# Kernel optimization log

Hardware: AMD Instinct MI355X
Metric: run time of the kernel (lower is better)

## Reference

```python
import jax, jax.numpy as jnp
import numpy as np

FREQ_DIM = 32
TIME_DIM = 32
HEADS = 8
TWO_PI = 6.283185307179586


def get_embeddings(B, H, W, freq_dim, time_dim, dtype):
    # freq embeddings over the height (frequency) axis
    nf = freq_dim // 2
    ln_x = jnp.log2(jnp.arange(0, H * nf, dtype=jnp.float32))
    ln_x = ln_x.at[0].set(-2.0)
    ln_x = ln_x.reshape(H, nf).T  # [nf, H]
    ln_x = ln_x * jnp.arange(1, nf + 1, dtype=jnp.float32)[:, None]
    # view_as_real(exp(1j*theta)) -> (cos, sin), interleaved per order along channel dim
    freq = jnp.stack([jnp.cos(ln_x), jnp.sin(ln_x)], axis=1).reshape(freq_dim, H)  # [freq_dim, H]
    freq = jnp.broadcast_to(freq[None, :, :, None], (B, freq_dim, H, W))

    # time embeddings over the width (time) axis
    nt = time_dim // 2
    k = jnp.arange(0, nt, dtype=jnp.float32) + 0.5  # [nt]
    x = jnp.arange(0, nt * W, dtype=jnp.float32).reshape(W, nt).T  # [nt, W]
    theta = k[:, None] * x / (W * nt) * TWO_PI  # [nt, W]
    time = jnp.stack([jnp.cos(theta), jnp.sin(theta)], axis=1).reshape(time_dim, W)  # [time_dim, W]
    time = jnp.broadcast_to(time[None, :, None, :], (B, time_dim, H, W))

    return jnp.concatenate([freq, time], axis=1).astype(dtype)  # [B, freq_dim+time_dim, H, W]


def setup_inputs() -> dict:
    key = jax.random.key(0)
    ks = jax.random.split(key, 6)
    B, C, H, W = 2, 512, 64, 32
    qkC = C + FREQ_DIM + TIME_DIM  # 576
    inner = HEADS * 64  # 512
    return {
        "hidden_states": jax.random.normal(ks[0], (B, C, H, W), dtype=jnp.float32),
        "Wq": jax.random.normal(ks[1], (qkC, inner), dtype=jnp.float32) * 0.02,
        "Wk": jax.random.normal(ks[2], (qkC, inner), dtype=jnp.float32) * 0.02,
        "Wv": jax.random.normal(ks[3], (C, inner), dtype=jnp.float32) * 0.02,
        "Wout": jax.random.normal(ks[4], (inner, C), dtype=jnp.float32) * 0.02,
        "bout": jnp.zeros((C,), dtype=jnp.float32),
    }


def reference(hidden_states, Wq, Wk, Wv, Wout, bout):
    B, C, H, W = hidden_states.shape
    emb = get_embeddings(B, H, W, FREQ_DIM, TIME_DIM, hidden_states.dtype)
    qk_hs = jnp.concatenate([hidden_states, emb], axis=1)  # [B, qkC, H, W]

    S = H * W
    qk_hs = qk_hs.reshape(B, -1, S).transpose(0, 2, 1)  # [B, S, qkC]
    v_hs = hidden_states.reshape(B, C, S).transpose(0, 2, 1)  # [B, S, C]

    q = qk_hs @ Wq  # [B, S, inner]
    k = qk_hs @ Wk
    v = v_hs @ Wv

    hd_qk = q.shape[-1] // HEADS
    hd_v = v.shape[-1] // HEADS
    q = q.reshape(B, S, HEADS, hd_qk).transpose(0, 2, 1, 3)  # [B, h, S, d]
    k = k.reshape(B, S, HEADS, hd_qk).transpose(0, 2, 1, 3)
    v = v.reshape(B, S, HEADS, hd_v).transpose(0, 2, 1, 3)

    scale = 1.0 / jnp.sqrt(jnp.asarray(hd_qk, dtype=q.dtype))
    scores = jnp.einsum('bhqd,bhkd->bhqk', q, k) * scale
    attn = jax.nn.softmax(scores, axis=-1)
    o = jnp.einsum('bhqk,bhkd->bhqd', attn, v)  # [B, h, S, d_v]

    o = o.transpose(0, 2, 1, 3).reshape(B, S, HEADS * hd_v)
    o = o @ Wout + bout  # [B, S, C]
    o = o.transpose(0, 2, 1).reshape(B, C, H, W)

    return o + hidden_states  # residual_connection=True, rescale_output_factor=1.0
```

## Files before the change

kernel.cpp:

```cpp
#include <hip/hip_runtime.h>
#include <math.h>

#define B_    2
#define C_    512
#define H_    64
#define W_    32
#define S_    2048
#define QKC_  576
#define INNER_ 512
#define NH_   8
#define HD_   64
#define TWO_PI_ 6.283185307179586f

typedef __attribute__((ext_vector_type(8))) short bfrag;
typedef __attribute__((ext_vector_type(4))) float ffrag;
typedef __attribute__((ext_vector_type(16))) float f16v;

typedef __attribute__((address_space(1))) const unsigned int as1_u32;
typedef __attribute__((address_space(3))) unsigned int as3_u32;

__device__ __forceinline__ ushort f2bf(float f) {
    unsigned u = __builtin_bit_cast(unsigned, f);
    unsigned r = (u + 0x7FFFu + ((u >> 16) & 1u)) >> 16;
    return (ushort)r;
}

__device__ __forceinline__ f16v zero16() {
    f16v z;
    #pragma unroll
    for (int i = 0; i < 16; i++) z[i] = 0.f;
    return z;
}

#define GLD(gp_, lp_) __builtin_amdgcn_global_load_lds((as1_u32*)(gp_), (as3_u32*)(lp_), 16, 0, 0)

__global__ void k_trans_emb(const float* __restrict__ hid, ushort* __restrict__ X) {
    __shared__ float t[32][33];
    int b  = blockIdx.z;
    int s0 = blockIdx.x * 32, c0 = blockIdx.y * 32;
    int tx = threadIdx.x, ty = threadIdx.y;
    if (c0 < 512) {
        t[ty][tx] = hid[((size_t)b * C_ + (c0 + ty)) * S_ + s0 + tx];
        __syncthreads();
        X[((size_t)(b * S_ + s0 + ty)) * QKC_ + c0 + tx] = f2bf(t[tx][ty]);
    } else {
        int c = c0 - 512 + tx;
        int s = s0 + ty;
        int h = s >> 5, w = s & 31;
        float val;
        if (c < 32) {
            int f = c >> 1;
            int n = h * 16 + f;
            float lx = (n == 0) ? -2.0f : log2f((float)n);
            float arg = lx * (float)(f + 1);
            val = (c & 1) ? sinf(arg) : cosf(arg);
        } else {
            int tt = (c - 32) >> 1;
            float theta = ((float)tt + 0.5f) * (float)(w * 16 + tt) * (TWO_PI_ / 512.0f);
            val = (c & 1) ? sinf(theta) : cosf(theta);
        }
        X[(size_t)(b * S_ + s) * QKC_ + c0 + tx] = f2bf(val);
    }
}

__global__ void k_wtrans_all(const float* __restrict__ Wq, const float* __restrict__ Wk,
                             const float* __restrict__ Wv, const float* __restrict__ Wo,
                             ushort* __restrict__ Wqt, ushort* __restrict__ Wkt,
                             ushort* __restrict__ Wvt, ushort* __restrict__ Wot) {
    __shared__ float t[32][33];
    int z = blockIdx.z;
    const float* W; ushort* Wt; int K;
    if (z == 0)      { W = Wq; Wt = Wqt; K = QKC_; }
    else if (z == 1) { W = Wk; Wt = Wkt; K = QKC_; }
    else if (z == 2) { W = Wv; Wt = Wvt; K = C_; }
    else             { W = Wo; Wt = Wot; K = INNER_; }
    int k0 = blockIdx.x * 32, n0 = blockIdx.y * 32;
    if (k0 >= K) return;
    int tx = threadIdx.x, ty = threadIdx.y;
    t[ty][tx] = W[(size_t)(k0 + ty) * 512 + n0 + tx];
    __syncthreads();
    Wt[(size_t)(n0 + ty) * K + k0 + tx] = f2bf(t[tx][ty]);
}

#define GSTAGE(buf_, k0_) {                                                   \
    _Pragma("unroll")                                                         \
    for (int i_ = 0; i_ < 6; i_++)                                            \
        GLD(gp[i_] + (k0_), tl + (buf_) * 12288 + lo[i_]); }

__global__ __launch_bounds__(256, 3) void k_qkv(const ushort* __restrict__ X,
                                                const ushort* __restrict__ Wqt,
                                                const ushort* __restrict__ Wkt,
                                                const ushort* __restrict__ Wvt,
                                                ushort* __restrict__ Qb,
                                                ushort* __restrict__ Kbb,
                                                ushort* __restrict__ Vtg) {
    __shared__ ushort __attribute__((aligned(16))) tl[2 * 12288];

    int tid = threadIdx.x;
    int l = tid & 63, wv = tid >> 6;
    int wr = wv >> 1, wc = wv & 1;
    int n0 = blockIdx.x * 64, m0 = blockIdx.y * 128;
    int sel = n0 >> 9, n0l = n0 & 511;
    const ushort* Bt = (sel == 0) ? Wqt : (sel == 1) ? Wkt : Wvt;
    const int K = (sel < 2) ? QKC_ : C_;
    const int nst = K >> 6;
    int l15 = l & 15, lg = l >> 4;
    int swz = l15 & 7;

    const ushort* gp[6];
    unsigned lo[6];
    {
        int rsub = l >> 3;
        int clog = (l & 7) ^ rsub;
        #pragma unroll
        for (int i = 0; i < 6; i++) {
            int c = wv * 6 + i;
            lo[i] = c * 512;
            if (c < 16) gp[i] = X  + (size_t)(m0  + c * 8        + rsub) * QKC_ + clog * 8;
            else        gp[i] = Bt + (size_t)(n0l + (c - 16) * 8 + rsub) * K    + clog * 8;
        }
    }

    ffrag acc[4][2];
    #pragma unroll
    for (int i = 0; i < 4; i++)
        #pragma unroll
        for (int j = 0; j < 2; j++) acc[i][j] = (ffrag){0.f, 0.f, 0.f, 0.f};

    GSTAGE(0, 0);
    int cur = 0;
    for (int kt = 0; kt < nst; kt++) {
        __syncthreads();
        if (kt + 1 < nst) GSTAGE(cur ^ 1, (kt + 1) * 64);
        const ushort* As = tl + cur * 12288;
        const ushort* Bs = As + 8192;
        #pragma unroll
        for (int ks = 0; ks < 2; ks++) {
            int cl = ks * 4 + lg;
            int ch = (cl ^ swz) * 8;
            bfrag af[4], bf[2];
            #pragma unroll
            for (int mi = 0; mi < 4; mi++)
                af[mi] = *(const bfrag*)(As + (wr * 64 + mi * 16 + l15) * 64 + ch);
            #pragma unroll
            for (int nj = 0; nj < 2; nj++)
                bf[nj] = *(const bfrag*)(Bs + (wc * 32 + nj * 16 + l15) * 64 + ch);
            #pragma unroll
            for (int mi = 0; mi < 4; mi++)
                #pragma unroll
                for (int nj = 0; nj < 2; nj++)
                    acc[mi][nj] = __builtin_amdgcn_mfma_f32_16x16x32_bf16(af[mi], bf[nj], acc[mi][nj], 0, 0, 0);
        }
        cur ^= 1;
    }

    if (sel < 2) {
        ushort* Co = sel ? Kbb : Qb;
        #pragma unroll
        for (int mi = 0; mi < 4; mi++)
            #pragma unroll
            for (int nj = 0; nj < 2; nj++)
                #pragma unroll
                for (int r = 0; r < 4; r++) {
                    int row = m0 + wr * 64 + mi * 16 + lg * 4 + r;
                    int col = n0l + wc * 32 + nj * 16 + l15;
                    Co[(size_t)row * INNER_ + col] = f2bf(acc[mi][nj][r]);
                }
    } else {
        ushort (*Ct)[136] = (ushort(*)[136])tl;
        __syncthreads();
        #pragma unroll
        for (int mi = 0; mi < 4; mi++)
            #pragma unroll
            for (int nj = 0; nj < 2; nj++)
                #pragma unroll
                for (int r = 0; r < 4; r++)
                    Ct[wc * 32 + nj * 16 + l15][wr * 64 + mi * 16 + lg * 4 + r] = f2bf(acc[mi][nj][r]);
        __syncthreads();
        int b = m0 >> 11, s0m = m0 & 2047;
        #pragma unroll
        for (int p = 0; p < 4; p++) {
            int c = tid + p * 256;
            int rowc = c >> 4, mc = c & 15;
            uint4 v = *(uint4*)&Ct[rowc][mc * 8];
            *(uint4*)(Vtg + (((size_t)(b * 512 + n0l + rowc)) << 11) + s0m + mc * 8) = v;
        }
    }
}

__global__ __launch_bounds__(256, 2) void k_og(const ushort* __restrict__ Ob,
                                               const ushort* __restrict__ Wot,
                                               const float* __restrict__ bias,
                                               const float* __restrict__ hid,
                                               float* __restrict__ out) {
    __shared__ ushort __attribute__((aligned(16))) tl[2 * 12288];

    int tid = threadIdx.x;
    int l = tid & 63, wv = tid >> 6;
    int wr = wv >> 1, wc = wv & 1;
    int n0 = blockIdx.x * 64, m0 = blockIdx.y * 128;
    int l15 = l & 15, lg = l >> 4;
    int swz = l15 & 7;

    const ushort* gp[6];
    unsigned lo[6];
    {
        int rsub = l >> 3;
        int clog = (l & 7) ^ rsub;
        #pragma unroll
        for (int i = 0; i < 6; i++) {
            int c = wv * 6 + i;
            lo[i] = c * 512;
            if (c < 16) gp[i] = Ob  + (size_t)(m0 + c * 8        + rsub) * INNER_ + clog * 8;
            else        gp[i] = Wot + (size_t)(n0 + (c - 16) * 8 + rsub) * INNER_ + clog * 8;
        }
    }

    ffrag acc[4][2];
    #pragma unroll
    for (int i = 0; i < 4; i++)
        #pragma unroll
        for (int j = 0; j < 2; j++) acc[i][j] = (ffrag){0.f, 0.f, 0.f, 0.f};

    GSTAGE(0, 0);
    int cur = 0;
    for (int kt = 0; kt < 8; kt++) {
        __syncthreads();
        if (kt < 7) GSTAGE(cur ^ 1, (kt + 1) * 64);
        const ushort* As = tl + cur * 12288;
        const ushort* Bs = As + 8192;
        #pragma unroll
        for (int ks = 0; ks < 2; ks++) {
            int cl = ks * 4 + lg;
            int ch = (cl ^ swz) * 8;
            bfrag af[4], bf[2];
            #pragma unroll
            for (int mi = 0; mi < 4; mi++)
                af[mi] = *(const bfrag*)(As + (wr * 64 + mi * 16 + l15) * 64 + ch);
            #pragma unroll
            for (int nj = 0; nj < 2; nj++)
                bf[nj] = *(const bfrag*)(Bs + (wc * 32 + nj * 16 + l15) * 64 + ch);
            #pragma unroll
            for (int mi = 0; mi < 4; mi++)
                #pragma unroll
                for (int nj = 0; nj < 2; nj++)
                    acc[mi][nj] = __builtin_amdgcn_mfma_f32_16x16x32_bf16(af[mi], bf[nj], acc[mi][nj], 0, 0, 0);
        }
        cur ^= 1;
    }

    float (*Cf)[129] = (float(*)[129])tl;
    float bv[2];
    #pragma unroll
    for (int nj = 0; nj < 2; nj++) bv[nj] = bias[n0 + wc * 32 + nj * 16 + l15];
    __syncthreads();
    #pragma unroll
    for (int mi = 0; mi < 4; mi++)
        #pragma unroll
        for (int nj = 0; nj < 2; nj++)
            #pragma unroll
            for (int r = 0; r < 4; r++)
                Cf[wc * 32 + nj * 16 + l15][wr * 64 + mi * 16 + lg * 4 + r] = acc[mi][nj][r] + bv[nj];
    __syncthreads();
    int b = m0 >> 11, s0m = m0 & 2047;
    #pragma unroll
    for (int p = 0; p < 8; p++) {
        int f = p * 256 + tid;
        int c = f >> 5, sq = (f & 31) * 4;
        size_t o = (((size_t)(b * 512 + n0 + c)) << 11) + s0m + sq;
        float4 hv = *(const float4*)(hid + o);
        float4 cv = *(float4*)&Cf[c][sq];
        cv.x += hv.x; cv.y += hv.y; cv.z += hv.z; cv.w += hv.w;
        *(float4*)(out + o) = cv;
    }
}

#define CVTPK(dst, a, b) asm("v_cvt_pk_bf16_f32 %0, %1, %2" : "=v"(dst) : "v"(a), "v"(b))
#define SWAP32(a, b)     asm("v_permlane32_swap_b32 %0, %1" : "+v"(a), "+v"(b))

#define STAGE(buf_, kt_) {                                                    \
    const ushort* g_ = gsrc + (size_t)(kt_) * ktstride;                       \
    ushort* lp_ = ktv + (buf_) * 16384 + wv * 4096;                           \
    _Pragma("unroll")                                                         \
    for (int i_ = 0; i_ < 8; i_++)                                            \
        GLD(g_ + (size_t)i_ * istride, lp_ + i_ * 512); }

__global__ __launch_bounds__(256, 2) void k_attn(const ushort* __restrict__ Qf,
                                                 const ushort* __restrict__ Kf,
                                                 const ushort* __restrict__ Vtg,
                                                 ushort* __restrict__ Ob) {
    __shared__ ushort __attribute__((aligned(16))) ktv[2 * 4 * 4096];
    __shared__ float mlsh[2][2][2][32];

    const int qb = blockIdx.x, hd = blockIdx.y, b = blockIdx.z;
    const int tid = threadIdx.x;
    const int l = tid & 63, wv = tid >> 6;
    const int wp = wv >> 1, hh = wv & 1;
    const int l31 = l & 31, hi = l >> 5, swz = l31 & 7;
    const int hoff = hd * HD_;
    const int brow = b * S_ + qb * 64;

    bfrag qf[4];
    {
        const ushort* qp = Qf + (size_t)(brow + wp * 32 + l31) * INNER_ + hoff + hi * 8;
        #pragma unroll
        for (int ks = 0; ks < 4; ks++) qf[ks] = *(const bfrag*)(qp + ks * 16);
    }

    const int hv = wv >> 1, isV = wv & 1;
    const int rr = l >> 3;
    const int clog = (l & 7) ^ rr;
    const ushort* gsrc;
    size_t istride, ktstride;
    if (isV) {
        gsrc = Vtg + (size_t)(b * 512 + hoff + rr) * 2048 + hv * 1024 + clog * 8;
        istride = (size_t)8 * 2048;
        ktstride = 64;
    } else {
        gsrc = Kf + (size_t)(b * S_ + hv * 1024 + rr) * INNER_ + hoff + clog * 8;
        istride = (size_t)8 * INNER_;
        ktstride = (size_t)64 * INNER_;
    }

    STAGE(0, 0);

    float m_run = -INFINITY, l_run = 0.f;
    f16v acc0 = zero16(), acc1 = zero16();
    int cur = 0;

    for (int kt = 0; kt < 16; kt++) {
        __syncthreads();
        if (kt < 15) STAGE(cur ^ 1, kt + 1);

        const ushort* Kt  = ktv + cur * 16384 + hh * 8192;
        const ushort* Vtt = Kt + 4096;

        f16v sf0 = zero16(), sf1 = zero16();
        #pragma unroll
        for (int ks = 0; ks < 4; ks++) {
            int ch = ((ks * 2 + hi) ^ swz) * 8;
            bfrag k0 = *(const bfrag*)(Kt + l31 * 64 + ch);
            bfrag k1 = *(const bfrag*)(Kt + (l31 + 32) * 64 + ch);
            sf0 = __builtin_amdgcn_mfma_f32_32x32x16_bf16(k0, qf[ks], sf0, 0, 0, 0);
            sf1 = __builtin_amdgcn_mfma_f32_32x32x16_bf16(k1, qf[ks], sf1, 0, 0, 0);
        }

        float tm = -INFINITY;
        #pragma unroll
        for (int j = 0; j < 16; j++) { tm = fmaxf(tm, sf0[j]); tm = fmaxf(tm, sf1[j]); }
        tm = fmaxf(tm, __shfl_xor(tm, 32));
        if (!__all(tm <= m_run + 64.0f)) {
            float mn = fmaxf(m_run, tm);
            float corr = __expf((m_run - mn) * 0.125f);
            l_run *= corr;
            #pragma unroll
            for (int j = 0; j < 16; j++) { acc0[j] *= corr; acc1[j] *= corr; }
            m_run = mn;
        }
        float nm8 = -m_run * 0.125f;
        float ls = 0.f;
        #pragma unroll
        for (int j = 0; j < 16; j++) { float p = __expf(fmaf(sf0[j], 0.125f, nm8)); sf0[j] = p; ls += p; }
        #pragma unroll
        for (int j = 0; j < 16; j++) { float p = __expf(fmaf(sf1[j], 0.125f, nm8)); sf1[j] = p; ls += p; }
        ls += __shfl_xor(ls, 32);
        l_run += ls;

        #pragma unroll
        for (int s = 0; s < 2; s++) {
            unsigned A0, B0, A1, B1;
            CVTPK(A0, sf0[s * 8 + 0], sf0[s * 8 + 1]); CVTPK(B0, sf0[s * 8 + 4], sf0[s * 8 + 5]);
            SWAP32(A0, B0);
            CVTPK(A1, sf0[s * 8 + 2], sf0[s * 8 + 3]); CVTPK(B1, sf0[s * 8 + 6], sf0[s * 8 + 7]);
            SWAP32(A1, B1);
            uint4 u; u.x = A0; u.y = A1; u.z = B0; u.w = B1;
            bfrag pa = __builtin_bit_cast(bfrag, u);
            int ch = ((s * 2 + hi) ^ swz) * 8;
            bfrag v0 = *(const bfrag*)(Vtt + l31 * 64 + ch);
            bfrag v1 = *(const bfrag*)(Vtt + (l31 + 32) * 64 + ch);
            acc0 = __builtin_amdgcn_mfma_f32_32x32x16_bf16(v0, pa, acc0, 0, 0, 0);
            acc1 = __builtin_amdgcn_mfma_f32_32x32x16_bf16(v1, pa, acc1, 0, 0, 0);
        }
        #pragma unroll
        for (int s = 0; s < 2; s++) {
            unsigned A0, B0, A1, B1;
            CVTPK(A0, sf1[s * 8 + 0], sf1[s * 8 + 1]); CVTPK(B0, sf1[s * 8 + 4], sf1[s * 8 + 5]);
            SWAP32(A0, B0);
            CVTPK(A1, sf1[s * 8 + 2], sf1[s * 8 + 3]); CVTPK(B1, sf1[s * 8 + 6], sf1[s * 8 + 7]);
            SWAP32(A1, B1);
            uint4 u; u.x = A0; u.y = A1; u.z = B0; u.w = B1;
            bfrag pa = __builtin_bit_cast(bfrag, u);
            int ch = (((2 + s) * 2 + hi) ^ swz) * 8;
            bfrag v0 = *(const bfrag*)(Vtt + l31 * 64 + ch);
            bfrag v1 = *(const bfrag*)(Vtt + (l31 + 32) * 64 + ch);
            acc0 = __builtin_amdgcn_mfma_f32_32x32x16_bf16(v0, pa, acc0, 0, 0, 0);
            acc1 = __builtin_amdgcn_mfma_f32_32x32x16_bf16(v1, pa, acc1, 0, 0, 0);
        }

        cur ^= 1;
    }

    if (l < 32) { mlsh[wp][hh][0][l] = m_run; mlsh[wp][hh][1][l] = l_run; }
    __syncthreads();
    float mo  = mlsh[wp][hh ^ 1][0][l31];
    float lo_ = mlsh[wp][hh ^ 1][1][l31];
    float mn2 = fmaxf(m_run, mo);
    float cs  = __expf((m_run - mn2) * 0.125f);
    float co  = __expf((mo    - mn2) * 0.125f);
    float inv = 1.0f / (cs * l_run + co * lo_);

    float* cmb = (float*)ktv;
    if (hh == 0) {
        #pragma unroll
        for (int j = 0; j < 16; j++) {
            int d0 = (j & 3) + 8 * (j >> 2) + 4 * hi;
            cmb[wp * 2112 + d0 * 33 + l31]        = cs * acc0[j];
            cmb[wp * 2112 + (d0 + 32) * 33 + l31] = cs * acc1[j];
        }
    }
    __syncthreads();
    if (hh == 1) {
        #pragma unroll
        for (int j = 0; j < 16; j++) {
            int d0 = (j & 3) + 8 * (j >> 2) + 4 * hi;
            int i0 = wp * 2112 + d0 * 33 + l31;
            int i1 = wp * 2112 + (d0 + 32) * 33 + l31;
            cmb[i0] = (cmb[i0] + cs * acc0[j]) * inv;
            cmb[i1] = (cmb[i1] + cs * acc1[j]) * inv;
        }
    }
    __syncthreads();
    #pragma unroll
    for (int p2 = 0; p2 < 2; p2++) {
        int f = p2 * 256 + tid;
        int q = f >> 3, dc = f & 7;
        int wpp = q >> 5, ql = q & 31;
        bfrag ov;
        #pragma unroll
        for (int j2 = 0; j2 < 8; j2++)
            ov[j2] = (short)f2bf(cmb[wpp * 2112 + (dc * 8 + j2) * 33 + ql]);
        *(uint4*)(Ob + (size_t)(brow + q) * INNER_ + hoff + dc * 8) = __builtin_bit_cast(uint4, ov);
    }
}

extern "C" void kernel_launch(void* const* d_in, const int* in_sizes, int n_in,
                              void* d_out, int out_size, void* d_ws, size_t ws_size,
                              hipStream_t stream) {
    const float* hid  = (const float*)d_in[0];
    const float* Wq   = (const float*)d_in[1];
    const float* Wk   = (const float*)d_in[2];
    const float* Wv   = (const float*)d_in[3];
    const float* Wout = (const float*)d_in[4];
    const float* bout = (const float*)d_in[5];
    float* out = (float*)d_out;

    const int M = B_ * S_;
    char* w = (char*)d_ws;
    ushort* X    = (ushort*)w;                    w += (size_t)M * QKC_ * 2;
    ushort* Qb   = (ushort*)w;                    w += (size_t)M * INNER_ * 2;
    ushort* Kbb  = (ushort*)w;                    w += (size_t)M * INNER_ * 2;
    ushort* Vtg  = (ushort*)w;                    w += (size_t)M * INNER_ * 2;
    ushort* Ob   = (ushort*)w;                    w += (size_t)M * INNER_ * 2;
    ushort* Wqt  = (ushort*)w;                    w += (size_t)INNER_ * QKC_ * 2;
    ushort* Wkt  = (ushort*)w;                    w += (size_t)INNER_ * QKC_ * 2;
    ushort* Wvt  = (ushort*)w;                    w += (size_t)INNER_ * C_ * 2;
    ushort* Wot  = (ushort*)w;                    w += (size_t)C_ * INNER_ * 2;

    k_wtrans_all<<<dim3(18, 16, 4), dim3(32, 32), 0, stream>>>(Wq, Wk, Wv, Wout,
                                                               Wqt, Wkt, Wvt, Wot);
    k_trans_emb<<<dim3(S_ / 32, 18, B_), dim3(32, 32), 0, stream>>>(hid, X);

    k_qkv<<<dim3(24, M / 128), 256, 0, stream>>>(X, Wqt, Wkt, Wvt, Qb, Kbb, Vtg);

    k_attn<<<dim3(S_ / 64, NH_, B_), 256, 0, stream>>>(Qb, Kbb, Vtg, Ob);

    k_og<<<dim3(C_ / 64, M / 128), 256, 0, stream>>>(Ob, Wot, bout, hid, out);
}
```

Baseline: 68.25 us.

## Remap block IDs for XCD locality, raise MFMA priority, use raw exp2

The qkv, attention and output GEMM kernels now launch on 1D grids and remap the block ID so consecutive logical tiles land on the same XCD (id&7 striding). This is meant to improve L2 reuse of shared K/V and weight tiles. The attention kernel also raises wave priority around the MFMA sections with s_setprio. It also replaces __expf with direct v_exp_f32 on log2e-prescaled inputs, removing a multiply per exponential. The raw exp2 instruction skips denormal handling, which is a small precision risk.

```diff
diff --git a/kernel.cpp b/kernel.cpp
--- a/kernel.cpp
+++ b/kernel.cpp
@@ -33,6 +33,8 @@
 }
 
 #define GLD(gp_, lp_) __builtin_amdgcn_global_load_lds((as1_u32*)(gp_), (as3_u32*)(lp_), 16, 0, 0)
+#define EXPA(dst_, x_) asm("v_exp_f32 %0, %1" : "=v"(dst_) : "v"(x_))
+#define SC_LOG2E 0.18033688011f
 
 __global__ void k_trans_emb(const float* __restrict__ hid, ushort* __restrict__ X) {
     __shared__ float t[32][33];
@@ -99,7 +101,10 @@
     int tid = threadIdx.x;
     int l = tid & 63, wv = tid >> 6;
     int wr = wv >> 1, wc = wv & 1;
-    int n0 = blockIdx.x * 64, m0 = blockIdx.y * 128;
+    int bid = blockIdx.x;
+    int lgc = (bid & 7) * 96 + (bid >> 3);
+    int bx = lgc % 24, by = lgc / 24;
+    int n0 = bx * 64, m0 = by * 128;
     int sel = n0 >> 9, n0l = n0 & 511;
     const ushort* Bt = (sel == 0) ? Wqt : (sel == 1) ? Wkt : Wvt;
     const int K = (sel < 2) ? QKC_ : C_;
@@ -198,7 +203,10 @@
     int tid = threadIdx.x;
     int l = tid & 63, wv = tid >> 6;
     int wr = wv >> 1, wc = wv & 1;
-    int n0 = blockIdx.x * 64, m0 = blockIdx.y * 128;
+    int bid = blockIdx.x;
+    int lgc = (bid & 7) * 32 + (bid >> 3);
+    int bx = lgc & 7, by = lgc >> 3;
+    int n0 = bx * 64, m0 = by * 128;
     int l15 = l & 15, lg = l >> 4;
     int swz = l15 & 7;
 
@@ -292,7 +300,12 @@
     __shared__ ushort __attribute__((aligned(16))) ktv[2 * 4 * 4096];
     __shared__ float mlsh[2][2][2][32];
 
-    const int qb = blockIdx.x, hd = blockIdx.y, b = blockIdx.z;
+    const int id = blockIdx.x;
+    const int lgc = (id & 7) * 64 + (id >> 3);
+    const int qb = lgc & 31;
+    const int hb = lgc >> 5;
+    const int hd = hb & 7, b = hb >> 3;
+
     const int tid = threadIdx.x;
     const int l = tid & 63, wv = tid >> 6;
     const int wp = wv >> 1, hh = wv & 1;
@@ -336,6 +349,7 @@
         const ushort* Vtt = Kt + 4096;
 
         f16v sf0 = zero16(), sf1 = zero16();
+        __builtin_amdgcn_s_setprio(1);
         #pragma unroll
         for (int ks = 0; ks < 4; ks++) {
             int ch = ((ks * 2 + hi) ^ swz) * 8;
@@ -344,6 +358,7 @@
             sf0 = __builtin_amdgcn_mfma_f32_32x32x16_bf16(k0, qf[ks], sf0, 0, 0, 0);
             sf1 = __builtin_amdgcn_mfma_f32_32x32x16_bf16(k1, qf[ks], sf1, 0, 0, 0);
         }
+        __builtin_amdgcn_s_setprio(0);
 
         float tm = -INFINITY;
         #pragma unroll
@@ -351,21 +366,22 @@
         tm = fmaxf(tm, __shfl_xor(tm, 32));
         if (!__all(tm <= m_run + 64.0f)) {
             float mn = fmaxf(m_run, tm);
-            float corr = __expf((m_run - mn) * 0.125f);
+            float corr; EXPA(corr, (m_run - mn) * SC_LOG2E);
             l_run *= corr;
             #pragma unroll
             for (int j = 0; j < 16; j++) { acc0[j] *= corr; acc1[j] *= corr; }
             m_run = mn;
         }
-        float nm8 = -m_run * 0.125f;
+        float nm = -m_run * SC_LOG2E;
         float ls = 0.f;
         #pragma unroll
-        for (int j = 0; j < 16; j++) { float p = __expf(fmaf(sf0[j], 0.125f, nm8)); sf0[j] = p; ls += p; }
-        #pragma unroll
-        for (int j = 0; j < 16; j++) { float p = __expf(fmaf(sf1[j], 0.125f, nm8)); sf1[j] = p; ls += p; }
+        for (int j = 0; j < 16; j++) { float p; EXPA(p, fmaf(sf0[j], SC_LOG2E, nm)); sf0[j] = p; ls += p; }
+        #pragma unroll
+        for (int j = 0; j < 16; j++) { float p; EXPA(p, fmaf(sf1[j], SC_LOG2E, nm)); sf1[j] = p; ls += p; }
         ls += __shfl_xor(ls, 32);
         l_run += ls;
 
+        __builtin_amdgcn_s_setprio(1);
         #pragma unroll
         for (int s = 0; s < 2; s++) {
             unsigned A0, B0, A1, B1;
@@ -396,6 +412,7 @@
             acc0 = __builtin_amdgcn_mfma_f32_32x32x16_bf16(v0, pa, acc0, 0, 0, 0);
             acc1 = __builtin_amdgcn_mfma_f32_32x32x16_bf16(v1, pa, acc1, 0, 0, 0);
         }
+        __builtin_amdgcn_s_setprio(0);
 
         cur ^= 1;
     }
@@ -405,8 +422,9 @@
     float mo  = mlsh[wp][hh ^ 1][0][l31];
     float lo_ = mlsh[wp][hh ^ 1][1][l31];
     float mn2 = fmaxf(m_run, mo);
-    float cs  = __expf((m_run - mn2) * 0.125f);
-    float co  = __expf((mo    - mn2) * 0.125f);
+    float cs, co;
+    EXPA(cs, (m_run - mn2) * SC_LOG2E);
+    EXPA(co, (mo    - mn2) * SC_LOG2E);
     float inv = 1.0f / (cs * l_run + co * lo_);
 
     float* cmb = (float*)ktv;
@@ -470,9 +488,9 @@
                                                                Wqt, Wkt, Wvt, Wot);
     k_trans_emb<<<dim3(S_ / 32, 18, B_), dim3(32, 32), 0, stream>>>(hid, X);
 
-    k_qkv<<<dim3(24, M / 128), 256, 0, stream>>>(X, Wqt, Wkt, Wvt, Qb, Kbb, Vtg);
-
-    k_attn<<<dim3(S_ / 64, NH_, B_), 256, 0, stream>>>(Qb, Kbb, Vtg, Ob);
-
-    k_og<<<dim3(C_ / 64, M / 128), 256, 0, stream>>>(Ob, Wot, bout, hid, out);
-}
+    k_qkv<<<dim3(768), 256, 0, stream>>>(X, Wqt, Wkt, Wvt, Qb, Kbb, Vtg);
+
+    k_attn<<<dim3(512), 256, 0, stream>>>(Qb, Kbb, Vtg, Ob);
+
+    k_og<<<dim3(256), 256, 0, stream>>>(Ob, Wot, bout, hid, out);
+}
```

After: 65.92 us. 1.04x faster.
